# Performance work log

Measured on AMD Instinct MI355X. Metric: run time of the kernel, lower is better.

Reference implementation:

```python
import jax, jax.numpy as jnp
import numpy as np

B, T, D = 1, 2048, 2048
H, HD = 32, 64
HEAD_COUNTS = np.array([8, 6, 4, 4, 6, 4])  # reasoning, creativity, curiosity, emotional, memory, meta
NEG = -1e9


def rope_tables(seq_len, dim, dtype):
    inv_freq = 1.0 / (10000.0 ** (jnp.arange(0, dim, 2, dtype=jnp.float32) / dim))
    t = jnp.arange(seq_len, dtype=jnp.float32)
    freqs = jnp.outer(t, inv_freq)            # [T, dim/2]
    emb = jnp.concatenate([freqs, freqs], -1) # [T, dim]
    return jnp.cos(emb).astype(dtype), jnp.sin(emb).astype(dtype)


def rotate_half(x):
    x1, x2 = jnp.split(x, 2, axis=-1)
    return jnp.concatenate([-x2, x1], axis=-1)


def setup_inputs() -> dict:
    key = jax.random.key(0)
    ks = jax.random.split(key, 8)
    x = jax.random.normal(ks[0], (B, T, D), jnp.float32)
    mask = jnp.tril(jnp.ones((T, T), jnp.int32))[None, None]  # causal [1,1,T,T]
    context_bias = jax.random.normal(ks[1], (B, T, T), jnp.float32) * 0.02
    mod_weights = jax.random.uniform(ks[2], (B, 6), jnp.float32, 0.5, 1.5)
    Wq = jax.random.normal(ks[3], (D, D), jnp.float32) * 0.02
    Wk = jax.random.normal(ks[4], (D, D), jnp.float32) * 0.02
    Wv = jax.random.normal(ks[5], (D, D), jnp.float32) * 0.02
    Wo = jax.random.normal(ks[6], (D, D), jnp.float32) * 0.02
    temp_scales = jnp.ones((H,), jnp.float32)
    return {"x": x, "mask": mask, "context_bias": context_bias,
            "mod_weights": mod_weights, "Wq": Wq, "Wk": Wk, "Wv": Wv,
            "Wo": Wo, "temp_scales": temp_scales}


def reference(x, mask, context_bias, mod_weights, Wq, Wk, Wv, Wo, temp_scales):
    b, t, d = x.shape
    # projections (torch Linear: y = x @ W.T)
    Q = (x @ Wq.T).reshape(b, t, H, HD).transpose(0, 2, 1, 3)  # [B,H,T,HD]
    K = (x @ Wk.T).reshape(b, t, H, HD).transpose(0, 2, 1, 3)
    V = (x @ Wv.T).reshape(b, t, H, HD).transpose(0, 2, 1, 3)
    cos, sin = rope_tables(t, HD, x.dtype)
    cos, sin = cos[None, None], sin[None, None]
    Q = Q * cos + rotate_half(Q) * sin
    K = K * cos + rotate_half(K) * sin
    scale = (HD ** -0.5) * temp_scales.reshape(1, H, 1, 1)
    attn = jnp.einsum('bhqd,bhkd->bhqk', Q, K) * scale
    attn = jnp.where(mask == 0, NEG, attn)
    attn = attn + context_bias[:, None]
    # per-head module reweight: expand [B,6] -> [B,H]
    w = jnp.repeat(mod_weights, np.asarray(HEAD_COUNTS), axis=1, total_repeat_length=H)
    attn = attn * w[:, :, None, None]
    attn = jax.nn.softmax(attn, axis=-1)
    out = jnp.einsum('bhqk,bhkd->bhqd', attn, V)
    out = out.transpose(0, 2, 1, 3).reshape(b, t, d)
    return out @ Wo.T
```

## Files before the change

### kernel.cpp

```cpp
#include <hip/hip_runtime.h>
#include <hip/hip_bf16.h>
#include <cstdint>
#include <cstddef>

typedef __bf16 bf16;
typedef bf16 bf16x4 __attribute__((ext_vector_type(4)));
typedef bf16 bf16x8 __attribute__((ext_vector_type(8)));
typedef float f32x4 __attribute__((ext_vector_type(4)));

#define MFMA_BF16(a,b,c) __builtin_amdgcn_mfma_f32_16x16x32_bf16((a),(b),(c),0,0,0)

typedef __attribute__((address_space(1))) const void gvoid;
typedef __attribute__((address_space(3))) void svoid;
__device__ __forceinline__ void gload16(const bf16* g, bf16* l){
  __builtin_amdgcn_global_load_lds((gvoid*)g, (svoid*)l, 16, 0, 0);
}

__device__ __forceinline__ int head_group(int h){
  return (h<8)?0:(h<14)?1:(h<18)?2:(h<22)?3:(h<28)?4:5;
}

struct CvtArgs { const float* src[6]; bf16* dst[6]; };
__global__ __launch_bounds__(256) void cvt6_kernel(CvtArgs a, int n){
  const int z = blockIdx.y;
  const float* __restrict__ in = a.src[z];
  bf16* __restrict__ out = a.dst[z];
  int i = (blockIdx.x*256 + threadIdx.x)*8;
  if (i >= n) return;
  const float4* p = (const float4*)(in + i);
  float4 va = p[0], vb = p[1];
  bf16x8 o;
  o[0]=(bf16)va.x; o[1]=(bf16)va.y; o[2]=(bf16)va.z; o[3]=(bf16)va.w;
  o[4]=(bf16)vb.x; o[5]=(bf16)vb.y; o[6]=(bf16)vb.z; o[7]=(bf16)vb.w;
  *(bf16x8*)(out+i) = o;
}

__global__ __launch_bounds__(256) void rope_tab_kernel(float* __restrict__ cosT,
                                                       float* __restrict__ sinT){
  const int t = blockIdx.x*8 + (threadIdx.x>>5);
  const int i = threadIdx.x&31;
  float invf = powf(10000.0f, -((float)i)/32.0f);
  float ang = (float)t * invf;
  cosT[t*32+i] = cosf(ang);
  sinT[t*32+i] = sinf(ang);
}

__device__ __forceinline__ void gemm_core(const bf16* __restrict__ A,
                                          const bf16* __restrict__ B,
                                          int row0, int col0,
                                          f32x4 (&acc)[4][4]){
  __shared__ bf16 As[128*32];
  __shared__ bf16 Bs[128*32];
  const int tid  = threadIdx.x;
  const int wave = tid>>6, lane = tid&63;
  const int l16  = lane&15, lg = lane>>4;
  const int wr   = wave>>1, wc = wave&1;

  const bf16* Ag0 = A + (size_t)(row0 + wave*32      + (lane>>2))*2048 + (lane&3)*8;
  const bf16* Ag1 = A + (size_t)(row0 + wave*32 + 16 + (lane>>2))*2048 + (lane&3)*8;
  const bf16* Bg0 = B + (size_t)(col0 + wave*32      + (lane>>2))*2048 + (lane&3)*8;
  const bf16* Bg1 = B + (size_t)(col0 + wave*32 + 16 + (lane>>2))*2048 + (lane&3)*8;
  bf16* AsB0 = As + (wave*32     )*32;
  bf16* AsB1 = As + (wave*32 + 16)*32;
  bf16* BsB0 = Bs + (wave*32     )*32;
  bf16* BsB1 = Bs + (wave*32 + 16)*32;

  #pragma unroll
  for (int m=0;m<4;++m)
    #pragma unroll
    for (int n=0;n<4;++n)
      #pragma unroll
      for (int r=0;r<4;++r) acc[m][n][r] = 0.f;

  for (int kt=0; kt<64; ++kt){
    const int ko = kt*32;
    gload16(Ag0 + ko, AsB0);
    gload16(Ag1 + ko, AsB1);
    gload16(Bg0 + ko, BsB0);
    gload16(Bg1 + ko, BsB1);
    __syncthreads();
    bf16x8 af[4], bfr[4];
    #pragma unroll
    for (int m=0;m<4;++m) af[m]  = *(const bf16x8*)&As[(wr*64+m*16+l16)*32 + lg*8];
    #pragma unroll
    for (int n=0;n<4;++n) bfr[n] = *(const bf16x8*)&Bs[(wc*64+n*16+l16)*32 + lg*8];
    #pragma unroll
    for (int m=0;m<4;++m)
      #pragma unroll
      for (int n=0;n<4;++n)
        acc[m][n] = MFMA_BF16(af[m], bfr[n], acc[m][n]);
    __syncthreads();
  }
}

__global__ __launch_bounds__(256) void gemm_qkv_kernel(
    const bf16* __restrict__ A,
    const bf16* __restrict__ B0, const bf16* __restrict__ B1, const bf16* __restrict__ B2,
    bf16* __restrict__ Qs, bf16* __restrict__ Ks, bf16* __restrict__ Vt,
    const float* __restrict__ cosT, const float* __restrict__ sinT,
    const float* __restrict__ mw, const float* __restrict__ ts){
  const int z = blockIdx.z;
  const bf16* B = (z==0)?B0:((z==1)?B1:B2);
  const int row0 = blockIdx.y*128, col0 = blockIdx.x*128;

  f32x4 acc[4][4];
  gemm_core(A, B, row0, col0, acc);

  const int tid  = threadIdx.x;
  const int wave = tid>>6, lane = tid&63;
  const int l16  = lane&15, lg = lane>>4;
  const int wr   = wave>>1, wc = wave&1;
  const int h    = (col0 + wc*64) >> 6;

  if (z == 2){
    #pragma unroll
    for (int n=0;n<4;++n){
      const int d = n*16 + l16;
      #pragma unroll
      for (int m=0;m<4;++m){
        const int t0 = row0 + wr*64 + m*16 + lg*4;
        bf16x4 v;
        #pragma unroll
        for (int r=0;r<4;++r) v[r] = (bf16)acc[m][n][r];
        *(bf16x4*)&Vt[((size_t)h*64 + d)*2048 + t0] = v;
      }
    }
  } else {
    const float sc = (z==0) ? 0.125f*ts[h]*mw[head_group(h)] : 1.0f;
    bf16* Out = (z==0) ? Qs : Ks;
    #pragma unroll
    for (int m=0;m<4;++m){
      #pragma unroll
      for (int r=0;r<4;++r){
        const int t = row0 + wr*64 + m*16 + lg*4 + r;
        const float* ct = cosT + t*32;
        const float* st = sinT + t*32;
        bf16* dst = Out + ((size_t)h*2048 + t)*64;
        #pragma unroll
        for (int n=0;n<2;++n){
          const int i = n*16 + l16;
          const float c = ct[i], s = st[i];
          const float a1 = acc[m][n][r], a2 = acc[m][n+2][r];
          dst[i]    = (bf16)((a1*c - a2*s)*sc);
          dst[i+32] = (bf16)((a2*c + a1*s)*sc);
        }
      }
    }
  }
}

__global__ __launch_bounds__(256) void gemm_out_kernel(
    const bf16* __restrict__ A, const bf16* __restrict__ B, float* __restrict__ C){
  const int row0 = blockIdx.y*128, col0 = blockIdx.x*128;
  f32x4 acc[4][4];
  gemm_core(A, B, row0, col0, acc);
  const int tid  = threadIdx.x;
  const int wave = tid>>6, lane = tid&63;
  const int l16  = lane&15, lg = lane>>4;
  const int wr   = wave>>1, wc = wave&1;
  #pragma unroll
  for (int m=0;m<4;++m)
    #pragma unroll
    for (int n=0;n<4;++n)
      #pragma unroll
      for (int r=0;r<4;++r){
        size_t idx = (size_t)(row0 + wr*64 + m*16 + lg*4 + r)*2048
                   + col0 + wc*64 + n*16 + l16;
        C[idx] = acc[m][n][r];
      }
}

__global__ __launch_bounds__(512) void attn_kernel(
    const bf16* __restrict__ Qs, const bf16* __restrict__ Ks,
    const bf16* __restrict__ Vt, const bf16* __restrict__ biasb,
    const float* __restrict__ mw, bf16* __restrict__ attout){
  const int n  = blockIdx.x;
  const int h  = ((n>>8)<<4) | ((n>>4)&15);
  const int qt = (n&256) ? (n&15) : 15-(n&15);
  const int tid = threadIdx.x, wid = tid>>6, lane = tid&63;
  const int l16 = lane&15, lg = lane>>4;
  const float w_h = mw[head_group(h)];
  const int qbase = qt*128 + wid*16;
  const int qg0 = qbase + lg*4;
  const int qtop = qbase + 15;
  const int nkt = 2*qt + 2;

  __shared__ bf16 Kl[2][4096];
  __shared__ bf16 Vl[2][4096];
  __shared__ bf16 plds[8][16][72];

  const int srow = wid*8 + (lane>>3);
  const int sswz = ((lane&7) ^ (srow&7))<<3;
  const bf16* KgS = Ks + (size_t)h*2048*64 + srow*64 + sswz;
  const bf16* VgS = Vt + ((size_t)h*64 + srow)*2048 + sswz;

  const bf16* Qp = Qs + ((size_t)h*2048 + qbase + l16)*64 + lg*8;
  bf16x8 qf0 = *(const bf16x8*)Qp;
  bf16x8 qf1 = *(const bf16x8*)(Qp + 32);

  const bf16* Bg = biasb + (size_t)qg0*2048;

  f32x4 O[4];
  float l[4] = {0.f,0.f,0.f,0.f};
  #pragma unroll
  for (int c=0;c<4;++c)
    #pragma unroll
    for (int r=0;r<4;++r) O[c][r] = 0.f;

  int rK0[4], rK1[4];
  #pragma unroll
  for (int c=0;c<4;++c){
    const int row = c*16 + l16;
    rK0[c] = row*64 + (((lg  ) ^ (row&7))<<3);
    rK1[c] = row*64 + (((4+lg) ^ (row&7))<<3);
  }

  float bc[4][4];
  #pragma unroll
  for (int c=0;c<4;++c)
    #pragma unroll
    for (int r=0;r<4;++r)
      bc[c][r] = w_h * (float)Bg[(size_t)r*2048 + c*16 + l16] - 4.0f;

  gload16(KgS, &Kl[0][wid*512]);
  gload16(VgS, &Vl[0][wid*512]);
  __syncthreads();

  int cur = 0;
  for (int kt=0; kt<nkt; ++kt){
    const int k0 = kt*64;
    const bool more = (kt+1 < nkt);
    if (more){
      bf16* kd = cur ? &Kl[0][wid*512] : &Kl[1][wid*512];
      bf16* vd = cur ? &Vl[0][wid*512] : &Vl[1][wid*512];
      gload16(KgS + (size_t)(k0+64)*64, kd);
      gload16(VgS + (k0+64), vd);
    }
    float bn[4][4];
    const bool needb = more && (k0+64 <= qtop);
    if (needb){
      #pragma unroll
      for (int c=0;c<4;++c)
        #pragma unroll
        for (int r=0;r<4;++r)
          bn[c][r] = w_h * (float)Bg[(size_t)r*2048 + (k0+64) + c*16 + l16] - 4.0f;
    }

    if (k0 <= qtop){
      f32x4 S[4];
      #pragma unroll
      for (int c=0;c<4;++c)
        #pragma unroll
        for (int r=0;r<4;++r) S[c][r] = bc[c][r];

      __builtin_amdgcn_s_setprio(1);
      #pragma unroll
      for (int c=0;c<4;++c){
        bf16x8 kf0 = *(const bf16x8*)&Kl[cur][rK0[c]];
        bf16x8 kf1 = *(const bf16x8*)&Kl[cur][rK1[c]];
        S[c] = MFMA_BF16(qf0, kf0, S[c]);
        S[c] = MFMA_BF16(qf1, kf1, S[c]);
      }
      __builtin_amdgcn_s_setprio(0);

      if (k0 + 63 > qbase){
        #pragma unroll
        for (int c=0;c<4;++c){
          const int kg = k0 + c*16 + l16;
          #pragma unroll
          for (int r=0;r<4;++r){
            float p = __expf(S[c][r]);
            if (kg > qg0+r) p = 0.f;
            S[c][r] = p; l[r] += p;
          }
        }
      } else {
        #pragma unroll
        for (int c=0;c<4;++c)
          #pragma unroll
          for (int r=0;r<4;++r){
            const float p = __expf(S[c][r]);
            S[c][r] = p; l[r] += p;
          }
      }

      #pragma unroll
      for (int c=0;c<4;++c)
        #pragma unroll
        for (int r=0;r<4;++r)
          plds[wid][lg*4+r][c*16+l16] = (bf16)S[c][r];
      bf16x8 pf0 = *(const bf16x8*)&plds[wid][l16][lg*8];
      bf16x8 pf1 = *(const bf16x8*)&plds[wid][l16][lg*8+32];

      __builtin_amdgcn_s_setprio(1);
      #pragma unroll
      for (int c=0;c<4;++c){
        bf16x8 vf0 = *(const bf16x8*)&Vl[cur][rK0[c]];
        bf16x8 vf1 = *(const bf16x8*)&Vl[cur][rK1[c]];
        O[c] = MFMA_BF16(pf0, vf0, O[c]);
        O[c] = MFMA_BF16(pf1, vf1, O[c]);
      }
      __builtin_amdgcn_s_setprio(0);
    }

    if (needb){
      #pragma unroll
      for (int c=0;c<4;++c)
        #pragma unroll
        for (int r=0;r<4;++r) bc[c][r] = bn[c][r];
    }
    __syncthreads();
    cur ^= (int)more;
  }

  #pragma unroll
  for (int r=0;r<4;++r){
    float v = l[r];
    v += __shfl_xor(v,1);
    v += __shfl_xor(v,2);
    v += __shfl_xor(v,4);
    v += __shfl_xor(v,8);
    l[r] = 1.0f / v;
  }
  #pragma unroll
  for (int c=0;c<4;++c)
    #pragma unroll
    for (int r=0;r<4;++r)
      attout[(size_t)(qg0+r)*2048 + h*64 + c*16 + l16] = (bf16)(O[c][r]*l[r]);
}

extern "C" void kernel_launch(void* const* d_in, const int* in_sizes, int n_in,
                              void* d_out, int out_size, void* d_ws, size_t ws_size,
                              hipStream_t stream){
  const float* x    = (const float*)d_in[0];
  const float* bias = (const float*)d_in[2];
  const float* mw   = (const float*)d_in[3];
  const float* Wq   = (const float*)d_in[4];
  const float* Wk   = (const float*)d_in[5];
  const float* Wv   = (const float*)d_in[6];
  const float* Wo   = (const float*)d_in[7];
  const float* ts   = (const float*)d_in[8];
  float* out = (float*)d_out;

  const size_t SZ = (size_t)2048*2048;
  bf16* base = (bf16*)d_ws;
  bf16* xb   = base;
  bf16* Wqb  = base + 1*SZ;
  bf16* Wkb  = base + 2*SZ;
  bf16* Wvb  = base + 3*SZ;
  bf16* Wob  = base + 4*SZ;
  bf16* bb   = base + 5*SZ;
  bf16* Qsb  = base + 6*SZ;
  bf16* Ksb  = base + 7*SZ;
  bf16* Vtb  = base + 8*SZ;
  bf16* att  = base + 9*SZ;
  float* cosT = (float*)(base + 10*SZ);
  float* sinT = cosT + 2048*32;

  CvtArgs ca;
  ca.src[0]=x;  ca.src[1]=Wq;  ca.src[2]=Wk;  ca.src[3]=Wv;  ca.src[4]=Wo;  ca.src[5]=bias;
  ca.dst[0]=xb; ca.dst[1]=Wqb; ca.dst[2]=Wkb; ca.dst[3]=Wvb; ca.dst[4]=Wob; ca.dst[5]=bb;
  const int nb = (int)(SZ/8/256);
  cvt6_kernel<<<dim3(nb,6),256,0,stream>>>(ca, (int)SZ);
  rope_tab_kernel<<<256,256,0,stream>>>(cosT, sinT);
  gemm_qkv_kernel<<<dim3(16,16,3),256,0,stream>>>(xb, Wqb,Wkb,Wvb,
                                                  Qsb,Ksb,Vtb, cosT,sinT, mw,ts);
  attn_kernel<<<512,512,0,stream>>>(Qsb,Ksb,Vtb,bb,mw,att);
  gemm_out_kernel<<<dim3(16,16),256,0,stream>>>(att, Wob, out);
}
```

Before: 182.9 us.

## Split long causal attention rows across two blocks and combine partials

Query tiles in the upper half of the sequence now have their key range split across two blocks. Each block writes unnormalized fp32 output and row sums into reused workspace, and a new combine kernel sums the two partials and normalizes them. The aim is to balance the causal workload and fill more CUs, since the grid grows from 512 to 768 blocks. The cost is an extra kernel launch plus fp32 partial traffic. Summing partials without a max rescale relies on the fixed -4 offset that the existing softmax already uses.

```diff
diff --git a/kernel.cpp b/kernel.cpp
--- a/kernel.cpp
+++ b/kernel.cpp
@@ -173,17 +173,31 @@
 __global__ __launch_bounds__(512) void attn_kernel(
     const bf16* __restrict__ Qs, const bf16* __restrict__ Ks,
     const bf16* __restrict__ Vt, const bf16* __restrict__ biasb,
-    const float* __restrict__ mw, bf16* __restrict__ attout){
-  const int n  = blockIdx.x;
-  const int h  = ((n>>8)<<4) | ((n>>4)&15);
-  const int qt = (n&256) ? (n&15) : 15-(n&15);
+    const float* __restrict__ mw, bf16* __restrict__ attout,
+    float* __restrict__ Opart, float* __restrict__ lpart){
+  const int n = blockIdx.x;
+  int h, qt, half; bool partial;
+  if (n < 512){
+    qt   = 15 - (n>>6);
+    half = (n>>5)&1;
+    h    = ((n&7)<<2) | ((n>>3)&3);
+    partial = true;
+  } else {
+    const int m = n - 512;
+    qt   = 7 - (m>>5);
+    half = 0;
+    h    = ((m&7)<<2) | ((m>>3)&3);
+    partial = false;
+  }
+  const int lo  = partial ? half*(qt+1) : 0;
+  const int cnt = partial ? (qt+1) : (2*qt+2);
+
   const int tid = threadIdx.x, wid = tid>>6, lane = tid&63;
   const int l16 = lane&15, lg = lane>>4;
   const float w_h = mw[head_group(h)];
   const int qbase = qt*128 + wid*16;
   const int qg0 = qbase + lg*4;
   const int qtop = qbase + 15;
-  const int nkt = 2*qt + 2;
 
   __shared__ bf16 Kl[2][4096];
   __shared__ bf16 Vl[2][4096];
@@ -220,16 +234,16 @@
   for (int c=0;c<4;++c)
     #pragma unroll
     for (int r=0;r<4;++r)
-      bc[c][r] = w_h * (float)Bg[(size_t)r*2048 + c*16 + l16] - 4.0f;
-
-  gload16(KgS, &Kl[0][wid*512]);
-  gload16(VgS, &Vl[0][wid*512]);
+      bc[c][r] = w_h * (float)Bg[(size_t)r*2048 + lo*64 + c*16 + l16] - 4.0f;
+
+  gload16(KgS + (size_t)(lo*64)*64, &Kl[0][wid*512]);
+  gload16(VgS + lo*64, &Vl[0][wid*512]);
   __syncthreads();
 
   int cur = 0;
-  for (int kt=0; kt<nkt; ++kt){
+  for (int kt=lo; kt<lo+cnt; ++kt){
     const int k0 = kt*64;
-    const bool more = (kt+1 < nkt);
+    const bool more = (kt+1 < lo+cnt);
     if (more){
       bf16* kd = cur ? &Kl[0][wid*512] : &Kl[1][wid*512];
       bf16* vd = cur ? &Vl[0][wid*512] : &Vl[1][wid*512];
@@ -320,13 +334,55 @@
     v += __shfl_xor(v,2);
     v += __shfl_xor(v,4);
     v += __shfl_xor(v,8);
-    l[r] = 1.0f / v;
-  }
-  #pragma unroll
-  for (int c=0;c<4;++c)
-    #pragma unroll
-    for (int r=0;r<4;++r)
-      attout[(size_t)(qg0+r)*2048 + h*64 + c*16 + l16] = (bf16)(O[c][r]*l[r]);
+    l[r] = v;
+  }
+
+  if (partial){
+    float* Op = Opart + (size_t)half*1024*2048;
+    #pragma unroll
+    for (int c=0;c<4;++c)
+      #pragma unroll
+      for (int r=0;r<4;++r)
+        Op[(size_t)(qg0 + r - 1024)*2048 + h*64 + c*16 + l16] = O[c][r];
+    if (l16 == 0){
+      #pragma unroll
+      for (int r=0;r<4;++r)
+        lpart[half*32768 + h*1024 + (qg0 + r - 1024)] = l[r];
+    }
+  } else {
+    #pragma unroll
+    for (int r=0;r<4;++r) l[r] = 1.0f / l[r];
+    #pragma unroll
+    for (int c=0;c<4;++c)
+      #pragma unroll
+      for (int r=0;r<4;++r)
+        attout[(size_t)(qg0+r)*2048 + h*64 + c*16 + l16] = (bf16)(O[c][r]*l[r]);
+  }
+}
+
+__global__ __launch_bounds__(256) void attn_combine_kernel(
+    const float* __restrict__ Opart, const float* __restrict__ lpart,
+    bf16* __restrict__ attout){
+  const int row = blockIdx.x;
+  const int h   = threadIdx.x>>3;
+  const int c0  = (threadIdx.x&7)*8;
+  const float la = lpart[h*1024 + row];
+  const float lb = lpart[32768 + h*1024 + row];
+  const float inv = 1.0f/(la + lb);
+  const size_t off = (size_t)row*2048 + h*64 + c0;
+  const float4* A = (const float4*)(Opart + off);
+  const float4* B = (const float4*)(Opart + (size_t)1024*2048 + off);
+  float4 a0 = A[0], a1 = A[1], b0 = B[0], b1 = B[1];
+  bf16x8 o;
+  o[0] = (bf16)((a0.x+b0.x)*inv);
+  o[1] = (bf16)((a0.y+b0.y)*inv);
+  o[2] = (bf16)((a0.z+b0.z)*inv);
+  o[3] = (bf16)((a0.w+b0.w)*inv);
+  o[4] = (bf16)((a1.x+b1.x)*inv);
+  o[5] = (bf16)((a1.y+b1.y)*inv);
+  o[6] = (bf16)((a1.z+b1.z)*inv);
+  o[7] = (bf16)((a1.w+b1.w)*inv);
+  *(bf16x8*)&attout[(size_t)(1024+row)*2048 + h*64 + c0] = o;
 }
 
 extern "C" void kernel_launch(void* const* d_in, const int* in_sizes, int n_in,
@@ -356,6 +412,8 @@
   bf16* att  = base + 9*SZ;
   float* cosT = (float*)(base + 10*SZ);
   float* sinT = cosT + 2048*32;
+  float* Opart = (float*)xb;
+  float* lpart = (float*)Wkb;
 
   CvtArgs ca;
   ca.src[0]=x;  ca.src[1]=Wq;  ca.src[2]=Wk;  ca.src[3]=Wv;  ca.src[4]=Wo;  ca.src[5]=bias;
@@ -365,6 +423,7 @@
   rope_tab_kernel<<<256,256,0,stream>>>(cosT, sinT);
   gemm_qkv_kernel<<<dim3(16,16,3),256,0,stream>>>(xb, Wqb,Wkb,Wvb,
                                                   Qsb,Ksb,Vtb, cosT,sinT, mw,ts);
-  attn_kernel<<<512,512,0,stream>>>(Qsb,Ksb,Vtb,bb,mw,att);
+  attn_kernel<<<768,512,0,stream>>>(Qsb,Ksb,Vtb,bb,mw,att, Opart,lpart);
+  attn_combine_kernel<<<1024,256,0,stream>>>(Opart, lpart, att);
   gemm_out_kernel<<<dim3(16,16),256,0,stream>>>(att, Wob, out);
 }
```

Result: no change. 186.1 us (+1.7%).
